# Optimization experiments

Hardware: AMD Instinct MI355X
Metric: run time of the kernel (lower is better)

The kernel has to match this reference:

```python
import jax, jax.numpy as jnp
import numpy as np

NEG_SLOPE = 0.2  # PyG GATConv default negative_slope


def _gat_conv(h, src, dst, N, W, a_src, a_dst, b, heads):
    """PyG GATConv (eval mode, self-loops already in src/dst).
    h: [N, F_in], W: [F_in, heads*C], a_src/a_dst: [heads, C], b: [heads*C]."""
    C = W.shape[1] // heads
    hl = (h @ W).reshape(N, heads, C)                      # [N,H,C]
    al_s = jnp.einsum('nhc,hc->nh', hl, a_src)             # [N,H]
    al_d = jnp.einsum('nhc,hc->nh', hl, a_dst)             # [N,H]
    e = jax.nn.leaky_relu(al_s[src] + al_d[dst], NEG_SLOPE)  # [E,H]
    # segment softmax over incoming edges of each destination node
    m = jax.ops.segment_max(e, dst, num_segments=N)        # [N,H]
    ex = jnp.exp(e - m[dst])
    s = jax.ops.segment_sum(ex, dst, num_segments=N)
    alpha = ex / (s[dst] + 1e-16)                          # [E,H]
    out = jax.ops.segment_sum(hl[src] * alpha[:, :, None], dst, num_segments=N)
    return out.reshape(N, heads * C) + b


def setup_inputs() -> dict:
    key = jax.random.key(0)
    ks = jax.random.split(key, 16)
    N, E, D = 30000, 240000, 64
    NUM_ENT, NUM_REL, NUM_DRUGS = 100000, 64, 200
    sc = 0.1
    return {
        'x': jax.random.randint(ks[0], (N,), 0, NUM_ENT),
        'edge_index': jax.random.randint(ks[1], (2, E), 0, N),
        'edge_type': jax.random.randint(ks[2], (N,), 0, NUM_REL),
        'ent_emb': jax.random.normal(ks[3], (NUM_ENT, D), jnp.float32) * sc,
        'rel_emb': jax.random.normal(ks[4], (NUM_REL, D), jnp.float32) * sc,
        'W1': jax.random.normal(ks[5], (2 * D, 8 * D), jnp.float32) * sc,
        'att1_src': jax.random.normal(ks[6], (8, D), jnp.float32) * sc,
        'att1_dst': jax.random.normal(ks[7], (8, D), jnp.float32) * sc,
        'b1': jax.random.normal(ks[8], (8 * D,), jnp.float32) * sc,
        'W2': jax.random.normal(ks[9], (9 * D, D), jnp.float32) * sc,
        'att2_src': jax.random.normal(ks[10], (1, D), jnp.float32) * sc,
        'att2_dst': jax.random.normal(ks[11], (1, D), jnp.float32) * sc,
        'b2': jax.random.normal(ks[12], (D,), jnp.float32) * sc,
        'fc_w': jax.random.normal(ks[13], (D, NUM_DRUGS), jnp.float32) * sc,
        'fc_b': jax.random.normal(ks[14], (NUM_DRUGS,), jnp.float32) * sc,
    }


def reference(x, edge_index, edge_type, ent_emb, rel_emb, W1, att1_src, att1_dst, b1,
              W2, att2_src, att2_dst, b2, fc_w, fc_b):
    N = x.shape[0]
    loop = jnp.arange(N)
    src = jnp.concatenate([edge_index[0], loop])  # GATConv add_self_loops=True
    dst = jnp.concatenate([edge_index[1], loop])
    ent = ent_emb[x]                               # [N,D]
    rel = rel_emb[edge_type]                       # [N,D]
    h = jnp.concatenate([ent, rel], axis=-1)       # [N,2D]  (dropout is identity in eval)
    h = jax.nn.elu(_gat_conv(h, src, dst, N, W1, att1_src, att1_dst, b1, heads=8))  # [N,8D]
    h = jnp.concatenate([h, ent], axis=-1)         # [N,9D]
    h = jax.nn.elu(_gat_conv(h, src, dst, N, W2, att2_src, att2_dst, b2, heads=1))  # [N,D]
    g = jnp.mean(h, axis=0, keepdims=True)         # [1,D]
    return g @ fc_w + fc_b                         # [1,num_drugs]
```

## Files before the change

### kernel.cpp

```cpp
#include <hip/hip_runtime.h>
#include <math.h>

#define NEG_SLOPE 0.2f

typedef __attribute__((ext_vector_type(8))) short short8;
typedef __attribute__((ext_vector_type(4))) float f32x4;

__device__ __forceinline__ float lrelu(float v) { return v > 0.f ? v : NEG_SLOPE * v; }
__device__ __forceinline__ float elu(float v) { return v > 0.f ? v : (__expf(v) - 1.f); }
__device__ __forceinline__ unsigned short f2b(float f) {
    unsigned u = __float_as_uint(f);
    return (unsigned short)((u + 0x7FFFu + ((u >> 16) & 1u)) >> 16);
}
__device__ __forceinline__ float blo(unsigned v) { return __uint_as_float(v << 16); }
__device__ __forceinline__ float bhi(unsigned v) { return __uint_as_float(v & 0xFFFF0000u); }
__device__ __forceinline__ unsigned packb(float a, float b) {
    return ((unsigned)f2b(b) << 16) | (unsigned)f2b(a);
}
__device__ __forceinline__ int sw(int r, int o) { return (o ^ (r & 7)) << 3; }

__global__ void prep_k(const int* __restrict__ x, const int* __restrict__ et,
                       const int* __restrict__ ei,
                       const float* __restrict__ ent_emb, const float* __restrict__ rel_emb,
                       const float* __restrict__ W1, const float* __restrict__ W2,
                       const float* __restrict__ a1s, const float* __restrict__ a1d,
                       unsigned short* __restrict__ h1b, unsigned short* __restrict__ wsb,
                       unsigned short* __restrict__ W1t, unsigned short* __restrict__ W2t,
                       int* __restrict__ deg, int N, int E) {
    int t = blockIdx.x * blockDim.x + threadIdx.x;
    if (t < N * 128) {
        int n = t >> 7, j = t & 127;
        float v = (j < 64) ? ent_emb[(size_t)x[n] * 64 + j]
                           : rel_emb[(size_t)et[n] * 64 + (j - 64)];
        h1b[t] = f2b(v);
    }
    if (t < 2048) {
        int hh = t >> 7, k = t & 127;
        int h = hh & 7;
        const float* aw = (hh < 8) ? a1s : a1d;
        const float* wr = W1 + (size_t)k * 512 + h * 64;
        float s_ = 0.f;
#pragma unroll 16
        for (int c = 0; c < 64; c++) s_ += wr[c] * aw[h * 64 + c];
        wsb[t] = f2b(s_);
    }
    if (t < 512 * 128) {
        int n = t >> 7, kk = t & 127;
        W1t[t] = f2b(W1[(size_t)kk * 512 + n]);
    }
    if (t < 64 * 576) {
        int n = t / 576, k = t % 576;
        W2t[t] = f2b(W2[(size_t)k * 64 + n]);
    }
    if (t < E + N) {
        int dst = t < E ? ei[E + t] : t - E;
        atomicAdd(&deg[dst], 1);
    }
}

__global__ __launch_bounds__(256) void attn1_k(const unsigned short* __restrict__ A,
                                               const unsigned short* __restrict__ Bt,
                                               float* __restrict__ als, float* __restrict__ ald,
                                               int M) {
    __shared__ __align__(16) unsigned short As[128 * 128];
    __shared__ __align__(16) unsigned short Bs[16 * 128];
    int tid = threadIdx.x;
    int m0 = blockIdx.x * 128;
    for (int c = tid; c < 2048; c += 256) {
        int r = c >> 4, o = c & 15;
        int gr = m0 + r;
        uint4 v = make_uint4(0u, 0u, 0u, 0u);
        if (gr < M) v = *(const uint4*)(A + (size_t)gr * 128 + o * 8);
        *(uint4*)(As + r * 128 + sw(r, o)) = v;
    }
    if (tid < 256) {
        int r = tid >> 4, o = tid & 15;
        uint4 v = *(const uint4*)(Bt + (size_t)r * 128 + o * 8);
        *(uint4*)(Bs + r * 128 + sw(r, o)) = v;
    }
    __syncthreads();
    int w = tid >> 6, lane = tid & 63;
    int wr = w * 32;
    int m16 = lane & 15, quad = lane >> 4;
    f32x4 acc[2] = {};
#pragma unroll
    for (int kk = 0; kk < 128; kk += 32) {
        int ob = (kk >> 3) + quad;
        short8 b = *(const short8*)(Bs + m16 * 128 + sw(m16, ob));
#pragma unroll
        for (int i = 0; i < 2; i++) {
            int r = wr + i * 16 + m16;
            short8 a = *(const short8*)(As + r * 128 + sw(r, ob));
            acc[i] = __builtin_amdgcn_mfma_f32_16x16x32_bf16(a, b, acc[i], 0, 0, 0);
        }
    }
#pragma unroll
    for (int i = 0; i < 2; i++)
#pragma unroll
        for (int reg = 0; reg < 4; reg++) {
            int row = m0 + wr + i * 16 + quad * 4 + reg;
            if (row < M) {
                if (m16 < 8) als[row * 8 + m16] = acc[i][reg];
                else         ald[row * 8 + (m16 - 8)] = acc[i][reg];
            }
        }
}

__global__ __launch_bounds__(256) void scanA_k(const int* __restrict__ deg,
                                               int* __restrict__ bsum, int N) {
    __shared__ int red[256];
    int t = threadIdx.x;
    int i = blockIdx.x * 256 + t;
    red[t] = (i < N) ? deg[i] : 0;
    __syncthreads();
    for (int off = 128; off > 0; off >>= 1) {
        if (t < off) red[t] += red[t + off];
        __syncthreads();
    }
    if (t == 0) bsum[blockIdx.x] = red[0];
}
__global__ void scanB_k(const int* __restrict__ bsum, int* __restrict__ bbase,
                        int* __restrict__ offs, int NB, int N, int Etot) {
    if (threadIdx.x == 0) {
        int run = 0;
        for (int i = 0; i < NB; i++) { bbase[i] = run; run += bsum[i]; }
        offs[N] = Etot;
    }
}
__global__ __launch_bounds__(256) void scanC_k(const int* __restrict__ deg,
                                               const int* __restrict__ bbase,
                                               int* __restrict__ offs, int N) {
    __shared__ int s[256];
    int t = threadIdx.x;
    int i = blockIdx.x * 256 + t;
    int v = (i < N) ? deg[i] : 0;
    s[t] = v;
    __syncthreads();
    for (int off = 1; off < 256; off <<= 1) {
        int tmp = (t >= off) ? s[t - off] : 0;
        __syncthreads();
        s[t] += tmp;
        __syncthreads();
    }
    if (i < N) offs[i] = bbase[blockIdx.x] + s[t] - v;
}

__global__ void fill_k(const int* __restrict__ ei, int E, int N,
                       const int* __restrict__ offs, int* __restrict__ cursor,
                       int* __restrict__ csr) {
    int e = blockIdx.x * blockDim.x + threadIdx.x;
    if (e >= E + N) return;
    int src = e < E ? ei[e] : e - E;
    int dst = e < E ? ei[E + e] : e - E;
    int pos = offs[dst] + atomicAdd(&cursor[dst], 1);
    csr[pos] = src;
}

__global__ __launch_bounds__(64) void aggG_k(const unsigned* __restrict__ h1u,
                                             const float* __restrict__ als1,
                                             const float* __restrict__ ald1,
                                             const int* __restrict__ offs,
                                             const int* __restrict__ csr,
                                             unsigned* __restrict__ Gu,
                                             unsigned* __restrict__ h2u, int N) {
    int n = blockIdx.x;
    int t = threadIdx.x;
    int hh = t & 7;
    float dl = ald1[n * 8 + hh];
    int p0 = offs[n], p1 = offs[n + 1];
    float a0[8] = {}, a1[8] = {};
    float ssacc = 0.f;
    for (int p = p0; p < p1; p++) {
        int src = csr[p];
        float x = __expf(lrelu(als1[src * 8 + hh] + dl));
        ssacc += x;
        unsigned hv = h1u[(size_t)src * 64 + t];
        float f0 = blo(hv), f1 = bhi(hv);
        float ev[8];
#pragma unroll
        for (int h = 0; h < 8; h++) ev[h] = __shfl(x, h, 64);
#pragma unroll
        for (int h = 0; h < 8; h++) {
            a0[h] += ev[h] * f0;
            a1[h] += ev[h] * f1;
        }
    }
#pragma unroll
    for (int h = 0; h < 8; h++) {
        float iv = 1.f / (__shfl(ssacc, h, 64) + 1e-16f);
        Gu[(size_t)n * 512 + h * 64 + t] = packb(a0[h] * iv, a1[h] * iv);
    }
    if (t < 32)
        h2u[(size_t)n * 288 + 256 + t] = h1u[(size_t)n * 64 + t];
}

__global__ __launch_bounds__(256) void gemmG_k(const unsigned short* __restrict__ Gb,
                                               const unsigned short* __restrict__ W1t,
                                               const float* __restrict__ b1,
                                               unsigned short* __restrict__ h2, int M) {
    __shared__ __align__(16) unsigned short As[128 * 128];
    __shared__ __align__(16) unsigned short Bs[64 * 128];
    int tid = threadIdx.x;
    int m0 = blockIdx.x * 128, h = blockIdx.y;
    for (int c = tid; c < 2048; c += 256) {
        int r = c >> 4, o = c & 15;
        int gr = m0 + r;
        uint4 v = make_uint4(0u, 0u, 0u, 0u);
        if (gr < M) v = *(const uint4*)(Gb + (size_t)gr * 1024 + h * 128 + o * 8);
        *(uint4*)(As + r * 128 + sw(r, o)) = v;
    }
    for (int c = tid; c < 1024; c += 256) {
        int r = c >> 4, o = c & 15;
        uint4 v = *(const uint4*)(W1t + (size_t)(h * 64 + r) * 128 + o * 8);
        *(uint4*)(Bs + r * 128 + sw(r, o)) = v;
    }
    __syncthreads();
    int w = tid >> 6, lane = tid & 63;
    int wr = w * 32;
    int m16 = lane & 15, quad = lane >> 4;
    f32x4 acc[2][4] = {};
#pragma unroll
    for (int kk = 0; kk < 128; kk += 32) {
        int ob = (kk >> 3) + quad;
        short8 b[4];
#pragma unroll
        for (int j = 0; j < 4; j++) {
            int r = j * 16 + m16;
            b[j] = *(const short8*)(Bs + r * 128 + sw(r, ob));
        }
#pragma unroll
        for (int i = 0; i < 2; i++) {
            int r = wr + i * 16 + m16;
            short8 a = *(const short8*)(As + r * 128 + sw(r, ob));
#pragma unroll
            for (int j = 0; j < 4; j++)
                acc[i][j] = __builtin_amdgcn_mfma_f32_16x16x32_bf16(a, b[j], acc[i][j], 0, 0, 0);
        }
    }
#pragma unroll
    for (int i = 0; i < 2; i++)
#pragma unroll
        for (int j = 0; j < 4; j++)
#pragma unroll
            for (int reg = 0; reg < 4; reg++) {
                int row = m0 + wr + i * 16 + quad * 4 + reg;
                int col = h * 64 + j * 16 + m16;
                if (row < M) h2[(size_t)row * 576 + col] = f2b(elu(acc[i][j][reg] + b1[col]));
            }
}

__global__ __launch_bounds__(256) void gemm2_k(const unsigned short* __restrict__ A,
                                               const unsigned short* __restrict__ Bt,
                                               unsigned short* __restrict__ Cb, int M) {
    __shared__ __align__(16) unsigned short As[128 * 64];
    __shared__ __align__(16) unsigned short Bs[64 * 64];
    int tid = threadIdx.x;
    int m0 = blockIdx.x * 128;
    int w = tid >> 6, lane = tid & 63;
    int wr = (w >> 1) * 64, wc = (w & 1) * 32;
    int m16 = lane & 15, quad = lane >> 4;
    f32x4 acc[4][2] = {};
    for (int k0 = 0; k0 < 576; k0 += 64) {
        __syncthreads();
        for (int c = tid; c < 1024; c += 256) {
            int r = c >> 3, o = c & 7;
            int gr = m0 + r;
            uint4 v = make_uint4(0u, 0u, 0u, 0u);
            if (gr < M) v = *(const uint4*)(A + (size_t)gr * 576 + k0 + o * 8);
            *(uint4*)(As + r * 64 + sw(r, o)) = v;
        }
        for (int c = tid; c < 512; c += 256) {
            int r = c >> 3, o = c & 7;
            uint4 v = *(const uint4*)(Bt + (size_t)r * 576 + k0 + o * 8);
            *(uint4*)(Bs + r * 64 + sw(r, o)) = v;
        }
        __syncthreads();
#pragma unroll
        for (int kk = 0; kk < 64; kk += 32) {
            int ob = (kk >> 3) + quad;
            short8 b[2];
#pragma unroll
            for (int j = 0; j < 2; j++) {
                int r = wc + j * 16 + m16;
                b[j] = *(const short8*)(Bs + r * 64 + sw(r, ob));
            }
#pragma unroll
            for (int i = 0; i < 4; i++) {
                int r = wr + i * 16 + m16;
                short8 a = *(const short8*)(As + r * 64 + sw(r, ob));
#pragma unroll
                for (int j = 0; j < 2; j++)
                    acc[i][j] = __builtin_amdgcn_mfma_f32_16x16x32_bf16(a, b[j], acc[i][j], 0, 0, 0);
            }
        }
    }
#pragma unroll
    for (int i = 0; i < 4; i++)
#pragma unroll
        for (int j = 0; j < 2; j++)
#pragma unroll
            for (int reg = 0; reg < 4; reg++) {
                int row = m0 + wr + i * 16 + quad * 4 + reg;
                int col = wc + j * 16 + m16;
                if (row < M) Cb[(size_t)row * 64 + col] = f2b(acc[i][j][reg]);
            }
}

__global__ void attn2_k(const unsigned short* __restrict__ hl, const float* __restrict__ aw_s,
                        const float* __restrict__ aw_d, float* __restrict__ als,
                        float* __restrict__ ald, int N) {
    int t = blockIdx.x * blockDim.x + threadIdx.x;
    if (t >= N) return;
    const unsigned short* row = hl + (size_t)t * 64;
    float s_ = 0.f, d_ = 0.f;
#pragma unroll
    for (int c = 0; c < 64; c += 2) {
        unsigned v = *(const unsigned*)(row + c);
        float f0 = blo(v), f1 = bhi(v);
        s_ += f0 * aw_s[c] + f1 * aw_s[c + 1];
        d_ += f0 * aw_d[c] + f1 * aw_d[c + 1];
    }
    als[t] = s_;
    ald[t] = d_;
}

__global__ __launch_bounds__(256) void agg2_k(const unsigned short* __restrict__ hl2,
                                              const float* __restrict__ als2,
                                              const float* __restrict__ ald2,
                                              const float* __restrict__ b2,
                                              const int* __restrict__ offs,
                                              const int* __restrict__ csr,
                                              float* __restrict__ gpart, int N) {
    __shared__ float red[512];
    int slot = threadIdx.x >> 5, l = threadIdx.x & 31;
    int n = blockIdx.x * 8 + slot;
    float v0 = 0.f, v1 = 0.f;
    if (n < N) {
        float dl = ald2[n];
        int p0 = offs[n], p1 = offs[n + 1];
        float a0 = 0.f, a1 = 0.f, ssum = 0.f;
        for (int p = p0; p < p1; p++) {
            int src = csr[p];
            float xv = __expf(lrelu(als2[src] + dl));
            ssum += xv;
            unsigned v = *(const unsigned*)(hl2 + (size_t)src * 64 + 2 * l);
            a0 += xv * blo(v);
            a1 += xv * bhi(v);
        }
        float inv = 1.f / (ssum + 1e-16f);
        v0 = elu(a0 * inv + b2[2 * l]);
        v1 = elu(a1 * inv + b2[2 * l + 1]);
    }
    red[slot * 64 + 2 * l] = v0;
    red[slot * 64 + 2 * l + 1] = v1;
    __syncthreads();
    if (threadIdx.x < 64) {
        float s = 0.f;
#pragma unroll
        for (int ss = 0; ss < 8; ss++) s += red[ss * 64 + threadIdx.x];
        gpart[(size_t)blockIdx.x * 64 + threadIdx.x] = s;
    }
}

__global__ __launch_bounds__(256) void colred_k(const float* __restrict__ gpart,
                                                float* __restrict__ gsum, int NBL) {
    __shared__ float red[256];
    int t = threadIdx.x;
    int c = t & 63, rg = t >> 6;
    int bend = blockIdx.x * 256 + 256; if (bend > NBL) bend = NBL;
    float acc = 0.f;
    for (int b = blockIdx.x * 256 + rg; b < bend; b += 4)
        acc += gpart[(size_t)b * 64 + c];
    red[t] = acc;
    __syncthreads();
    if (t < 64) atomicAdd(&gsum[c], red[c] + red[c + 64] + red[c + 128] + red[c + 192]);
}

__global__ __launch_bounds__(256) void final_k(const float* __restrict__ gsum,
                                               const float* __restrict__ fcw,
                                               const float* __restrict__ fcb,
                                               float* __restrict__ out, int N) {
    __shared__ float g[64];
    int t = threadIdx.x;
    if (t < 64) g[t] = gsum[t] / (float)N;
    __syncthreads();
    if (t < 200) {
        float acc = fcb[t];
#pragma unroll
        for (int c = 0; c < 64; c++) acc += g[c] * fcw[c * 200 + t];
        out[t] = acc;
    }
}

extern "C" void kernel_launch(void* const* d_in, const int* in_sizes, int n_in,
                              void* d_out, int out_size, void* d_ws, size_t ws_size,
                              hipStream_t stream) {
    const int* x = (const int*)d_in[0];
    const int* ei = (const int*)d_in[1];
    const int* et = (const int*)d_in[2];
    const float* ent_emb = (const float*)d_in[3];
    const float* rel_emb = (const float*)d_in[4];
    const float* W1 = (const float*)d_in[5];
    const float* a1s = (const float*)d_in[6];
    const float* a1d = (const float*)d_in[7];
    const float* b1 = (const float*)d_in[8];
    const float* W2 = (const float*)d_in[9];
    const float* a2s = (const float*)d_in[10];
    const float* a2d = (const float*)d_in[11];
    const float* b2 = (const float*)d_in[12];
    const float* fcw = (const float*)d_in[13];
    const float* fcb = (const float*)d_in[14];
    float* out = (float*)d_out;

    int N = in_sizes[0];
    int E = in_sizes[1] / 2;
    int Etot = E + N;
    int NB = (N + 255) / 256;
    int NBL = (N + 7) / 8;

    char* p = (char*)d_ws;
    auto alloc = [&](size_t bytes) -> char* {
        char* r = p;
        p += (bytes + 255) & ~(size_t)255;
        return r;
    };
    unsigned short* h1b = (unsigned short*)alloc((size_t)N * 128 * 2);
    unsigned short* wsb = (unsigned short*)alloc(2048 * 2);
    unsigned short* W1t = (unsigned short*)alloc((size_t)512 * 128 * 2);
    unsigned short* W2t = (unsigned short*)alloc((size_t)64 * 576 * 2);
    float* als1 = (float*)alloc((size_t)N * 8 * 4);
    float* ald1 = (float*)alloc((size_t)N * 8 * 4);
    unsigned* Gu = (unsigned*)alloc((size_t)N * 512 * 4);
    unsigned short* h2  = (unsigned short*)alloc((size_t)N * 576 * 2);
    unsigned short* hl2 = (unsigned short*)alloc((size_t)N * 64 * 2);
    float* als2 = (float*)alloc((size_t)N * 4);
    float* ald2 = (float*)alloc((size_t)N * 4);
    float* gpart = (float*)alloc((size_t)NBL * 64 * 4);
    int* offs   = (int*)alloc((size_t)(N + 1) * 4);
    int* csr    = (int*)alloc((size_t)Etot * 4);
    int* bsum   = (int*)alloc((size_t)NB * 4);
    int* bbase  = (int*)alloc((size_t)NB * 4);
    char* z0 = p;
    int* deg    = (int*)alloc((size_t)N * 4);
    int* cursor = (int*)alloc((size_t)N * 4);
    float* gsum = (float*)alloc(64 * 4);
    size_t zbytes = (size_t)(p - z0);

    int tb = 256;
    hipMemsetAsync(z0, 0, zbytes, stream);
    prep_k<<<(N * 128 + tb - 1) / tb, tb, 0, stream>>>(x, et, ei, ent_emb, rel_emb, W1, W2,
                                                       a1s, a1d, h1b, wsb, W1t, W2t, deg, N, E);
    attn1_k<<<(N + 127) / 128, 256, 0, stream>>>(h1b, wsb, als1, ald1, N);
    scanA_k<<<NB, 256, 0, stream>>>(deg, bsum, N);
    scanB_k<<<1, 64, 0, stream>>>(bsum, bbase, offs, NB, N, Etot);
    scanC_k<<<NB, 256, 0, stream>>>(deg, bbase, offs, N);
    fill_k<<<(Etot + tb - 1) / tb, tb, 0, stream>>>(ei, E, N, offs, cursor, csr);
    aggG_k<<<N, 64, 0, stream>>>((const unsigned*)h1b, als1, ald1, offs, csr, Gu, (unsigned*)h2, N);
    gemmG_k<<<dim3((N + 127) / 128, 8), 256, 0, stream>>>((const unsigned short*)Gu, W1t, b1, h2, N);
    gemm2_k<<<(N + 127) / 128, 256, 0, stream>>>(h2, W2t, hl2, N);
    attn2_k<<<(N + tb - 1) / tb, tb, 0, stream>>>(hl2, a2s, a2d, als2, ald2, N);
    agg2_k<<<NBL, 256, 0, stream>>>(hl2, als2, ald2, b2, offs, csr, gpart, N);
    colred_k<<<(NBL + 255) / 256, 256, 0, stream>>>(gpart, gsum, NBL);
    final_k<<<1, 256, 0, stream>>>(gsum, fcw, fcb, out, N);
}
```

Baseline: 282.2 us.

## Cut kernel launches: fused scan, fused gemm2+attn2, fused final reduction, init kernel

Replaces the memset with an init kernel that zeroes state and prepares the weights, splitting weight prep out of the large prep kernel. The three-kernel scan becomes one decoupled-lookback scan. Attention logits for layer 2 are computed in the gemm2 epilogue, with gemm2 retiled to 64-row blocks. The column reduction and final FC merge into one kernel using a last-block counter. The aim is to remove launch and pass overhead, at the cost of spin-waiting across blocks in the scan and fewer rows per gemm2 block.

```diff
diff --git a/kernel.cpp b/kernel.cpp
--- a/kernel.cpp
+++ b/kernel.cpp
@@ -19,38 +19,47 @@
 }
 __device__ __forceinline__ int sw(int r, int o) { return (o ^ (r & 7)) << 3; }
 
+__global__ __launch_bounds__(256) void init_k(int* __restrict__ zbase, int zwords,
+                                              const float* __restrict__ W1,
+                                              const float* __restrict__ W2,
+                                              const float* __restrict__ a1s,
+                                              const float* __restrict__ a1d,
+                                              unsigned short* __restrict__ wsb,
+                                              unsigned short* __restrict__ W1t,
+                                              unsigned short* __restrict__ W2t) {
+    int t = blockIdx.x * blockDim.x + threadIdx.x;
+    int stride = gridDim.x * blockDim.x;
+    for (int i = t; i < zwords; i += stride) zbase[i] = 0;
+    for (int i = t; i < 2048; i += stride) {
+        int hh = i >> 7, k = i & 127, h = hh & 7;
+        const float* aw = (hh < 8) ? a1s : a1d;
+        const float* wr = W1 + (size_t)k * 512 + h * 64;
+        float s_ = 0.f;
+#pragma unroll 16
+        for (int c = 0; c < 64; c++) s_ += wr[c] * aw[h * 64 + c];
+        wsb[i] = f2b(s_);
+    }
+    for (int i = t; i < 512 * 128; i += stride) {
+        int n = i >> 7, kk = i & 127;
+        W1t[i] = f2b(W1[(size_t)kk * 512 + n]);
+    }
+    for (int i = t; i < 64 * 576; i += stride) {
+        int n = i / 576, k = i % 576;
+        W2t[i] = f2b(W2[(size_t)k * 64 + n]);
+    }
+}
+
 __global__ void prep_k(const int* __restrict__ x, const int* __restrict__ et,
                        const int* __restrict__ ei,
                        const float* __restrict__ ent_emb, const float* __restrict__ rel_emb,
-                       const float* __restrict__ W1, const float* __restrict__ W2,
-                       const float* __restrict__ a1s, const float* __restrict__ a1d,
-                       unsigned short* __restrict__ h1b, unsigned short* __restrict__ wsb,
-                       unsigned short* __restrict__ W1t, unsigned short* __restrict__ W2t,
-                       int* __restrict__ deg, int N, int E) {
+                       unsigned short* __restrict__ h1b, int* __restrict__ deg,
+                       int N, int E) {
     int t = blockIdx.x * blockDim.x + threadIdx.x;
     if (t < N * 128) {
         int n = t >> 7, j = t & 127;
         float v = (j < 64) ? ent_emb[(size_t)x[n] * 64 + j]
                            : rel_emb[(size_t)et[n] * 64 + (j - 64)];
         h1b[t] = f2b(v);
-    }
-    if (t < 2048) {
-        int hh = t >> 7, k = t & 127;
-        int h = hh & 7;
-        const float* aw = (hh < 8) ? a1s : a1d;
-        const float* wr = W1 + (size_t)k * 512 + h * 64;
-        float s_ = 0.f;
-#pragma unroll 16
-        for (int c = 0; c < 64; c++) s_ += wr[c] * aw[h * 64 + c];
-        wsb[t] = f2b(s_);
-    }
-    if (t < 512 * 128) {
-        int n = t >> 7, kk = t & 127;
-        W1t[t] = f2b(W1[(size_t)kk * 512 + n]);
-    }
-    if (t < 64 * 576) {
-        int n = t / 576, k = t % 576;
-        W2t[t] = f2b(W2[(size_t)k * 64 + n]);
     }
     if (t < E + N) {
         int dst = t < E ? ei[E + t] : t - E;
@@ -106,33 +115,14 @@
         }
 }
 
-__global__ __launch_bounds__(256) void scanA_k(const int* __restrict__ deg,
-                                               int* __restrict__ bsum, int N) {
-    __shared__ int red[256];
-    int t = threadIdx.x;
-    int i = blockIdx.x * 256 + t;
-    red[t] = (i < N) ? deg[i] : 0;
-    __syncthreads();
-    for (int off = 128; off > 0; off >>= 1) {
-        if (t < off) red[t] += red[t + off];
-        __syncthreads();
-    }
-    if (t == 0) bsum[blockIdx.x] = red[0];
-}
-__global__ void scanB_k(const int* __restrict__ bsum, int* __restrict__ bbase,
-                        int* __restrict__ offs, int NB, int N, int Etot) {
-    if (threadIdx.x == 0) {
-        int run = 0;
-        for (int i = 0; i < NB; i++) { bbase[i] = run; run += bsum[i]; }
-        offs[N] = Etot;
-    }
-}
-__global__ __launch_bounds__(256) void scanC_k(const int* __restrict__ deg,
-                                               const int* __restrict__ bbase,
-                                               int* __restrict__ offs, int N) {
+__global__ __launch_bounds__(256) void scan_k(const int* __restrict__ deg,
+                                              int* __restrict__ offs,
+                                              int* __restrict__ bstate,
+                                              int N, int Etot, int NB) {
     __shared__ int s[256];
-    int t = threadIdx.x;
-    int i = blockIdx.x * 256 + t;
+    __shared__ int sbase;
+    int b = blockIdx.x, t = threadIdx.x;
+    int i = b * 256 + t;
     int v = (i < N) ? deg[i] : 0;
     s[t] = v;
     __syncthreads();
@@ -142,7 +132,28 @@
         s[t] += tmp;
         __syncthreads();
     }
-    if (i < N) offs[i] = bbase[blockIdx.x] + s[t] - v;
+    int total = s[255];
+    if (t == 0) {
+        if (b == 0) {
+            atomicExch(&bstate[0], (total << 2) | 2);
+            sbase = 0;
+        } else {
+            atomicExch(&bstate[b], (total << 2) | 1);
+            int run = 0;
+            for (int p = b - 1; p >= 0;) {
+                int stv;
+                do { stv = atomicAdd(&bstate[p], 0); } while ((stv & 3) == 0);
+                run += (stv >> 2);
+                if ((stv & 3) == 2) break;
+                p--;
+            }
+            atomicExch(&bstate[b], ((run + total) << 2) | 2);
+            sbase = run;
+        }
+    }
+    __syncthreads();
+    if (i < N) offs[i] = sbase + s[t] - v;
+    if (b == NB - 1 && t == 0) offs[N] = Etot;
 }
 
 __global__ void fill_k(const int* __restrict__ ei, int E, int N,
@@ -251,18 +262,21 @@
 
 __global__ __launch_bounds__(256) void gemm2_k(const unsigned short* __restrict__ A,
                                                const unsigned short* __restrict__ Bt,
-                                               unsigned short* __restrict__ Cb, int M) {
-    __shared__ __align__(16) unsigned short As[128 * 64];
+                                               const float* __restrict__ a2s,
+                                               const float* __restrict__ a2d,
+                                               unsigned short* __restrict__ Cb,
+                                               float* __restrict__ als2,
+                                               float* __restrict__ ald2, int M) {
+    __shared__ __align__(16) unsigned short As[64 * 64];
     __shared__ __align__(16) unsigned short Bs[64 * 64];
     int tid = threadIdx.x;
-    int m0 = blockIdx.x * 128;
+    int m0 = blockIdx.x * 64;
     int w = tid >> 6, lane = tid & 63;
-    int wr = (w >> 1) * 64, wc = (w & 1) * 32;
     int m16 = lane & 15, quad = lane >> 4;
-    f32x4 acc[4][2] = {};
+    f32x4 acc[4] = {};
     for (int k0 = 0; k0 < 576; k0 += 64) {
         __syncthreads();
-        for (int c = tid; c < 1024; c += 256) {
+        for (int c = tid; c < 512; c += 256) {
             int r = c >> 3, o = c & 7;
             int gr = m0 + r;
             uint4 v = make_uint4(0u, 0u, 0u, 0u);
@@ -278,50 +292,48 @@
 #pragma unroll
         for (int kk = 0; kk < 64; kk += 32) {
             int ob = (kk >> 3) + quad;
-            short8 b[2];
-#pragma unroll
-            for (int j = 0; j < 2; j++) {
-                int r = wc + j * 16 + m16;
-                b[j] = *(const short8*)(Bs + r * 64 + sw(r, ob));
+            int r = w * 16 + m16;
+            short8 a = *(const short8*)(As + r * 64 + sw(r, ob));
+#pragma unroll
+            for (int j = 0; j < 4; j++) {
+                int rb = j * 16 + m16;
+                short8 b = *(const short8*)(Bs + rb * 64 + sw(rb, ob));
+                acc[j] = __builtin_amdgcn_mfma_f32_16x16x32_bf16(a, b, acc[j], 0, 0, 0);
             }
-#pragma unroll
-            for (int i = 0; i < 4; i++) {
-                int r = wr + i * 16 + m16;
-                short8 a = *(const short8*)(As + r * 64 + sw(r, ob));
-#pragma unroll
-                for (int j = 0; j < 2; j++)
-                    acc[i][j] = __builtin_amdgcn_mfma_f32_16x16x32_bf16(a, b[j], acc[i][j], 0, 0, 0);
-            }
-        }
-    }
-#pragma unroll
-    for (int i = 0; i < 4; i++)
-#pragma unroll
-        for (int j = 0; j < 2; j++)
-#pragma unroll
-            for (int reg = 0; reg < 4; reg++) {
-                int row = m0 + wr + i * 16 + quad * 4 + reg;
-                int col = wc + j * 16 + m16;
-                if (row < M) Cb[(size_t)row * 64 + col] = f2b(acc[i][j][reg]);
-            }
-}
-
-__global__ void attn2_k(const unsigned short* __restrict__ hl, const float* __restrict__ aw_s,
-                        const float* __restrict__ aw_d, float* __restrict__ als,
-                        float* __restrict__ ald, int N) {
-    int t = blockIdx.x * blockDim.x + threadIdx.x;
-    if (t >= N) return;
-    const unsigned short* row = hl + (size_t)t * 64;
-    float s_ = 0.f, d_ = 0.f;
-#pragma unroll
-    for (int c = 0; c < 64; c += 2) {
-        unsigned v = *(const unsigned*)(row + c);
-        float f0 = blo(v), f1 = bhi(v);
-        s_ += f0 * aw_s[c] + f1 * aw_s[c + 1];
-        d_ += f0 * aw_d[c] + f1 * aw_d[c + 1];
-    }
-    als[t] = s_;
-    ald[t] = d_;
+        }
+    }
+#pragma unroll
+    for (int j = 0; j < 4; j++)
+#pragma unroll
+        for (int reg = 0; reg < 4; reg++) {
+            int row = m0 + w * 16 + quad * 4 + reg;
+            int col = j * 16 + m16;
+            if (row < M) Cb[(size_t)row * 64 + col] = f2b(acc[j][reg]);
+        }
+    float sa[4] = {}, sd[4] = {};
+#pragma unroll
+    for (int j = 0; j < 4; j++) {
+        int col = j * 16 + m16;
+        float as_ = a2s[col], ad_ = a2d[col];
+#pragma unroll
+        for (int reg = 0; reg < 4; reg++) {
+            sa[reg] += acc[j][reg] * as_;
+            sd[reg] += acc[j][reg] * ad_;
+        }
+    }
+#pragma unroll
+    for (int m = 1; m < 16; m <<= 1)
+#pragma unroll
+        for (int reg = 0; reg < 4; reg++) {
+            sa[reg] += __shfl_xor(sa[reg], m, 64);
+            sd[reg] += __shfl_xor(sd[reg], m, 64);
+        }
+    if (m16 == 0)
+#pragma unroll
+        for (int reg = 0; reg < 4; reg++) {
+            int row = m0 + w * 16 + quad * 4 + reg;
+            if (row < M) { als2[row] = sa[reg]; ald2[row] = sd[reg]; }
+        }
 }
 
 __global__ __launch_bounds__(256) void agg2_k(const unsigned short* __restrict__ hl2,
@@ -362,9 +374,15 @@
     }
 }
 
-__global__ __launch_bounds__(256) void colred_k(const float* __restrict__ gpart,
-                                                float* __restrict__ gsum, int NBL) {
+__global__ __launch_bounds__(256) void colredfinal_k(const float* __restrict__ gpart,
+                                                     float* __restrict__ gsum,
+                                                     int* __restrict__ done,
+                                                     const float* __restrict__ fcw,
+                                                     const float* __restrict__ fcb,
+                                                     float* __restrict__ out,
+                                                     int NBL, int N, int NCB) {
     __shared__ float red[256];
+    __shared__ int isLast;
     int t = threadIdx.x;
     int c = t & 63, rg = t >> 6;
     int bend = blockIdx.x * 256 + 256; if (bend > NBL) bend = NBL;
@@ -374,21 +392,22 @@
     red[t] = acc;
     __syncthreads();
     if (t < 64) atomicAdd(&gsum[c], red[c] + red[c + 64] + red[c + 128] + red[c + 192]);
-}
-
-__global__ __launch_bounds__(256) void final_k(const float* __restrict__ gsum,
-                                               const float* __restrict__ fcw,
-                                               const float* __restrict__ fcb,
-                                               float* __restrict__ out, int N) {
-    __shared__ float g[64];
-    int t = threadIdx.x;
-    if (t < 64) g[t] = gsum[t] / (float)N;
-    __syncthreads();
-    if (t < 200) {
-        float acc = fcb[t];
-#pragma unroll
-        for (int c = 0; c < 64; c++) acc += g[c] * fcw[c * 200 + t];
-        out[t] = acc;
+    __threadfence();
+    if (t == 0) {
+        int old = atomicAdd(done, 1);
+        isLast = (old == NCB - 1) ? 1 : 0;
+    }
+    __syncthreads();
+    if (isLast) {
+        __shared__ float g[64];
+        if (t < 64) g[t] = atomicAdd(&gsum[t], 0.f) / (float)N;
+        __syncthreads();
+        if (t < 200) {
+            float a = fcb[t];
+#pragma unroll
+            for (int cc = 0; cc < 64; cc++) a += g[cc] * fcw[cc * 200 + t];
+            out[t] = a;
+        }
     }
 }
 
@@ -417,6 +436,7 @@
     int Etot = E + N;
     int NB = (N + 255) / 256;
     int NBL = (N + 7) / 8;
+    int NCB = (NBL + 255) / 256;
 
     char* p = (char*)d_ws;
     auto alloc = [&](size_t bytes) -> char* {
@@ -438,28 +458,23 @@
     float* gpart = (float*)alloc((size_t)NBL * 64 * 4);
     int* offs   = (int*)alloc((size_t)(N + 1) * 4);
     int* csr    = (int*)alloc((size_t)Etot * 4);
-    int* bsum   = (int*)alloc((size_t)NB * 4);
-    int* bbase  = (int*)alloc((size_t)NB * 4);
     char* z0 = p;
     int* deg    = (int*)alloc((size_t)N * 4);
     int* cursor = (int*)alloc((size_t)N * 4);
     float* gsum = (float*)alloc(64 * 4);
-    size_t zbytes = (size_t)(p - z0);
+    int* done   = (int*)alloc(4);
+    int* bstate = (int*)alloc((size_t)NB * 4);
+    size_t zwords = (size_t)(p - z0) / 4;
 
     int tb = 256;
-    hipMemsetAsync(z0, 0, zbytes, stream);
-    prep_k<<<(N * 128 + tb - 1) / tb, tb, 0, stream>>>(x, et, ei, ent_emb, rel_emb, W1, W2,
-                                                       a1s, a1d, h1b, wsb, W1t, W2t, deg, N, E);
+    init_k<<<256, tb, 0, stream>>>((int*)z0, (int)zwords, W1, W2, a1s, a1d, wsb, W1t, W2t);
+    prep_k<<<(N * 128 + tb - 1) / tb, tb, 0, stream>>>(x, et, ei, ent_emb, rel_emb, h1b, deg, N, E);
     attn1_k<<<(N + 127) / 128, 256, 0, stream>>>(h1b, wsb, als1, ald1, N);
-    scanA_k<<<NB, 256, 0, stream>>>(deg, bsum, N);
-    scanB_k<<<1, 64, 0, stream>>>(bsum, bbase, offs, NB, N, Etot);
-    scanC_k<<<NB, 256, 0, stream>>>(deg, bbase, offs, N);
+    scan_k<<<NB, 256, 0, stream>>>(deg, offs, bstate, N, Etot, NB);
     fill_k<<<(Etot + tb - 1) / tb, tb, 0, stream>>>(ei, E, N, offs, cursor, csr);
     aggG_k<<<N, 64, 0, stream>>>((const unsigned*)h1b, als1, ald1, offs, csr, Gu, (unsigned*)h2, N);
     gemmG_k<<<dim3((N + 127) / 128, 8), 256, 0, stream>>>((const unsigned short*)Gu, W1t, b1, h2, N);
-    gemm2_k<<<(N + 127) / 128, 256, 0, stream>>>(h2, W2t, hl2, N);
-    attn2_k<<<(N + tb - 1) / tb, tb, 0, stream>>>(hl2, a2s, a2d, als2, ald2, N);
+    gemm2_k<<<(N + 63) / 64, 256, 0, stream>>>(h2, W2t, a2s, a2d, hl2, als2, ald2, N);
     agg2_k<<<NBL, 256, 0, stream>>>(hl2, als2, ald2, b2, offs, csr, gpart, N);
-    colred_k<<<(NBL + 255) / 256, 256, 0, stream>>>(gpart, gsum, NBL);
-    final_k<<<1, 256, 0, stream>>>(gsum, fcw, fcb, out, N);
-}
+    colredfinal_k<<<NCB, 256, 0, stream>>>(gpart, gsum, done, fcw, fcb, out, NBL, N, NCB);
+}
```

Measured after the change: 273.8 us. 3.0% less time.
